# Performance work log

Measured on AMD Instinct MI355X. Metric: run time of the kernel, lower is better.

The kernel has to match this reference:

```python
import jax, jax.numpy as jnp
import numpy as np

B, T, F, H = 4096, 48, 64, 128


def _uniform(key, shape, stdv):
    return jax.random.uniform(key, shape, jnp.float32, -stdv, stdv)


def setup_inputs() -> dict:
    key = jax.random.key(0)
    ks = jax.random.split(key, 24)
    values = jax.random.normal(ks[0], (B, T, F), jnp.float32)
    masks = (jax.random.uniform(ks[1], (B, T, F)) < 0.8).astype(jnp.float32)
    deltas = jax.random.uniform(ks[2], (B, T, F), jnp.float32)
    sH = 1.0 / np.sqrt(H)
    sF = 1.0 / np.sqrt(F)
    inp = {
        "values": values, "masks": masks, "deltas": deltas,
        # TemporalDecay h: W [H, F], b [H] (stdv = 1/sqrt(out=H))
        "Wdh": _uniform(ks[3], (H, F), sH), "bdh": _uniform(ks[4], (H,), sH),
        # TemporalDecay x (diag): W [F, F], b [F]
        "Wdx": _uniform(ks[5], (F, F), sF), "bdx": _uniform(ks[6], (F,), sF),
        # hist_reg: Linear(H -> F)
        "Wh": _uniform(ks[7], (F, H), sH), "bh": _uniform(ks[8], (F,), sH),
        # feat_reg: masked F x F
        "Wf": _uniform(ks[9], (F, F), sF), "bf": _uniform(ks[10], (F,), sF),
        # weight_combine: Linear(2F -> F)
        "Wc": _uniform(ks[11], (F, 2 * F), 1.0 / np.sqrt(2 * F)),
        "bc": _uniform(ks[12], (F,), 1.0 / np.sqrt(2 * F)),
        # LSTMCell(2F -> H): gates in PyTorch order i, f, g, o
        "W_ih": _uniform(ks[13], (4 * H, 2 * F), sH),
        "W_hh": _uniform(ks[14], (4 * H, H), sH),
        "b_ih": _uniform(ks[15], (4 * H,), sH),
        "b_hh": _uniform(ks[16], (4 * H,), sH),
        # out: Linear(H -> 1)
        "Wo": _uniform(ks[17], (1, H), sH), "bo": _uniform(ks[18], (1,), sH),
    }
    return inp


def reference(values, masks, deltas, Wdh, bdh, Wdx, bdx, Wh, bh, Wf, bf,
              Wc, bc, W_ih, W_hh, b_ih, b_hh, Wo, bo):
    impute_weight = 1.0
    b, t, f = values.shape
    h_dim = Wdh.shape[0]
    eye = jnp.eye(f, dtype=values.dtype)
    Wdx_m = Wdx * eye            # diagonal temporal decay
    Wf_m = Wf * (1.0 - eye)

    def step(carry, xt):
        h, c, loss = carry
        x, m, d = xt  # each [B, F]
        gamma_h = jnp.exp(-jax.nn.relu(d @ Wdh.T + bdh))        # [B, H]
        gamma_x = jnp.exp(-jax.nn.relu(d @ Wdx_m.T + bdx))      # [B, F]
        h = h * gamma_h
        x_h = h @ Wh.T + bh
        denom = jnp.sum(m) + 1e-5
        loss = loss + jnp.sum(jnp.abs(x - x_h) * m) / denom
        x_c = m * x + (1.0 - m) * x_h
        z_h = x_c @ Wf_m.T + bf
        loss = loss + jnp.sum(jnp.abs(x - z_h) * m) / denom
        alpha = jnp.concatenate([gamma_x, m], axis=1) @ Wc.T + bc
        c_h = alpha * z_h + (1.0 - alpha) * x_h
        loss = loss + jnp.sum(jnp.abs(x - c_h) * m) / denom
        c_c = m * x + (1.0 - m) * c_h
        inputs = jnp.concatenate([c_c, m], axis=1)  # [B, 2F]
        gates = inputs @ W_ih.T + b_ih + h @ W_hh.T + b_hh
        i_g, f_g, g_g, o_g = jnp.split(gates, 4, axis=1)
        c = jax.nn.sigmoid(f_g) * c + jax.nn.sigmoid(i_g) * jnp.tanh(g_g)
        h = jax.nn.sigmoid(o_g) * jnp.tanh(c)
        return (h, c, loss), c_c

    init = (jnp.zeros((b, h_dim), values.dtype),
            jnp.zeros((b, h_dim), values.dtype),
            jnp.zeros((), values.dtype))
    xs = (jnp.swapaxes(values, 0, 1),
          jnp.swapaxes(masks, 0, 1),
          jnp.swapaxes(deltas, 0, 1))
    (h, c, x_loss), imps = jax.lax.scan(step, init, xs)
    imputations = jnp.swapaxes(imps, 0, 1)  # [B, T, F]
    predictions = h @ Wo.T + bo             # [B, 1]
    return x_loss * impute_weight, imputations, predictions
```

## Files before the change

### kernel.cpp

```cpp
#include <hip/hip_runtime.h>
#include <hip/hip_bf16.h>
#include <math.h>

#define BB 4096
#define TT 48
#define FF 64
#define HH 128
#define ROWS 16
#define NT 1024
#define NBLK (BB / ROWS)

typedef __attribute__((ext_vector_type(8))) short short8;
typedef __attribute__((ext_vector_type(4))) float f32x4;

#define MFMA(a, b, c) __builtin_amdgcn_mfma_f32_16x16x32_bf16((a), (b), (c), 0, 0, 0)

__device__ __forceinline__ float sigm(float x) { return 1.f / (1.f + __expf(-x)); }
__device__ __forceinline__ float tanh_f(float x) { return 2.f / (1.f + __expf(-2.f * x)) - 1.f; }

__global__ __launch_bounds__(256) void prep_kernel(
    const float* __restrict__ W_ih, const float* __restrict__ W_hh,
    const float* __restrict__ Wdh,  const float* __restrict__ Wh,
    const float* __restrict__ Wf,   const float* __restrict__ Wc,
    __hip_bfloat16* __restrict__ frags) {
    const int idx = blockIdx.x * 256 + threadIdx.x;
    float v;
    if (idx < 131072) {
        const int jj = idx & 7;
        const int lane = (idx >> 3) & 63;
        const int ks = (idx >> 9) & 7;
        const int tile = idx >> 12;
        const int n = tile * 16 + (lane & 15);
        const int k = ks * 32 + ((lane >> 4) << 3) + jj;
        v = (k < 128) ? W_ih[n * 128 + k] : W_hh[n * 128 + (k - 128)];
    } else {
        const int u = idx - 131072;
        const int jj = u & 7;
        const int lane = (u >> 3) & 63;
        const int lq = lane & 15, q8 = (lane >> 4) << 3;
        if (u < 8192) {
            const int ks = (u >> 9) & 1, nt = u >> 10;
            const int n = nt * 16 + lq, k = ks * 32 + q8 + jj;
            v = Wdh[n * 64 + k];
        } else if (u < 16384) {
            const int uu = u - 8192;
            const int ks = (uu >> 9) & 3, nt = uu >> 11;
            const int n = nt * 16 + lq, k = ks * 32 + q8 + jj;
            v = Wh[n * 128 + k];
        } else if (u < 20480) {
            const int uu = u - 16384;
            const int ks = (uu >> 9) & 1, nt = uu >> 10;
            const int n = nt * 16 + lq, k = ks * 32 + q8 + jj;
            v = (k == n) ? 0.f : Wf[n * 64 + k];
        } else {
            const int uu = u - 20480;
            const int ks = (uu >> 9) & 3, nt = uu >> 11;
            const int n = nt * 16 + lq, k = ks * 32 + q8 + jj;
            v = Wc[n * 128 + k];
        }
    }
    frags[idx] = __float2bfloat16(v);
}

__global__ __launch_bounds__(256) void denom1_kernel(const float* __restrict__ masks,
                                                     float* __restrict__ partials) {
    const int t = blockIdx.x >> 5;
    const int s = blockIdx.x & 31;
    const int tid = threadIdx.x;
    float acc = 0.f;
    #pragma unroll
    for (int k = 0; k < 8; ++k) {
        const int i = k * 256 + tid;
        const int b = s * 128 + (i >> 4);
        const int f = (i & 15) << 2;
        const float4 v = *(const float4*)&masks[((size_t)b * TT + t) * FF + f];
        acc += v.x + v.y + v.z + v.w;
    }
    #pragma unroll
    for (int off = 32; off; off >>= 1) acc += __shfl_down(acc, off, 64);
    __shared__ float red[4];
    if ((tid & 63) == 0) red[tid >> 6] = acc;
    __syncthreads();
    if (tid == 0) partials[blockIdx.x] = red[0] + red[1] + red[2] + red[3];
}

__global__ __launch_bounds__(64) void denom2_kernel(const float* __restrict__ partials,
                                                    float* __restrict__ inv_denom) {
    const int t = threadIdx.x;
    if (t < TT) {
        float s = 0.f;
        #pragma unroll
        for (int i = 0; i < 32; ++i) s += partials[t * 32 + i];
        inv_denom[t] = 1.f / (s + 1e-5f);
    }
}

__global__ __launch_bounds__(NT) void rits_kernel(
    const float* __restrict__ values, const float* __restrict__ masks,
    const float* __restrict__ deltas,
    const float* __restrict__ Wdx, const float* __restrict__ bdx,
    const float* __restrict__ bdh, const float* __restrict__ bh,
    const float* __restrict__ bf,  const float* __restrict__ bc,
    const float* __restrict__ b_ih, const float* __restrict__ b_hh,
    const float* __restrict__ Wo,  const float* __restrict__ bo,
    const __hip_bfloat16* __restrict__ frags,
    const float* __restrict__ inv_denom,
    float* __restrict__ ws_lossblk,
    float* __restrict__ out_imp, float* __restrict__ out_pred)
{
    __shared__ short8 whh_frag[8192];
    __shared__ __hip_bfloat16 dbuf[ROWS][72];
    __shared__ __hip_bfloat16 gxbuf[ROWS][72];
    __shared__ __hip_bfloat16 mbuf[ROWS][72];
    __shared__ __hip_bfloat16 xcbuf[ROWS][72];
    __shared__ __hip_bfloat16 ccbuf[ROWS][72];
    __shared__ __hip_bfloat16 hbufB[ROWS][136];
    __shared__ float x_lds[ROWS][65];
    __shared__ float m_lds[ROWS][65];
    __shared__ float albuf[ROWS][68];
    __shared__ float redl[16];

    const int tid = threadIdx.x;
    const int bid = blockIdx.x;
    const int b0 = bid * ROWS;
    const int lane = tid & 63;
    const int wv = tid >> 6;
    const int quad = lane >> 4;
    const int lq = lane & 15;

    const short8* f8 = (const short8*)frags;

    for (int i = tid; i < 8192; i += NT) {
        const int slot = i >> 6, ln = i & 63;
        const int g = slot >> 5, rem = slot & 31, j = rem >> 2, kk = rem & 3;
        whh_frag[i] = f8[(((g * 8 + j) * 8 + 4 + kk) << 6) + ln];
    }
    for (int i = tid; i < ROWS * 136; i += NT) ((unsigned short*)hbufB)[i] = 0;
    __syncthreads();

    float loss_acc = 0.f;

    if (wv < 8) {
        const int j_ln = wv * 16 + lq;
        const float bdh_w = bdh[j_ln];
        const float bI = b_ih[j_ln]       + b_hh[j_ln];
        const float bF = b_ih[128 + j_ln] + b_hh[128 + j_ln];
        const float bG = b_ih[256 + j_ln] + b_hh[256 + j_ln];
        const float bO = b_ih[384 + j_ln] + b_hh[384 + j_ln];
        short8 Bgam[2];
        #pragma unroll
        for (int ks = 0; ks < 2; ++ks) Bgam[ks] = f8[16384 + ((wv * 2 + ks) << 6) + lane];
        const int wbase = (wv << 8) + lane;
        const int gbase = (wv << 9) + lane;

        float c_reg[4], h_reg[4];
        #pragma unroll
        for (int r = 0; r < 4; ++r) { c_reg[r] = 0.f; h_reg[r] = 0.f; }

        __syncthreads();
        for (int t = 0; t < TT; ++t) {
            short8 Bm[4][2];
            #pragma unroll
            for (int g = 0; g < 4; ++g)
                #pragma unroll
                for (int kk = 0; kk < 2; ++kk)
                    Bm[g][kk] = f8[gbase + (g << 12) + ((2 + kk) << 6)];
            f32x4 gacc0 = {0.f,0.f,0.f,0.f}, gacc1 = {0.f,0.f,0.f,0.f};
            f32x4 gacc2 = {0.f,0.f,0.f,0.f}, gacc3 = {0.f,0.f,0.f,0.f};
            #pragma unroll
            for (int kk = 0; kk < 4; ++kk) {
                const short8 a = *(const short8*)&hbufB[lq][kk * 32 + quad * 8];
                gacc0 = MFMA(a, whh_frag[wbase + 0    + kk * 64], gacc0);
                gacc1 = MFMA(a, whh_frag[wbase + 2048 + kk * 64], gacc1);
                gacc2 = MFMA(a, whh_frag[wbase + 4096 + kk * 64], gacc2);
                gacc3 = MFMA(a, whh_frag[wbase + 6144 + kk * 64], gacc3);
            }
            __syncthreads();

            short8 Bcc[4][2];
            #pragma unroll
            for (int g = 0; g < 4; ++g)
                #pragma unroll
                for (int kk = 0; kk < 2; ++kk)
                    Bcc[g][kk] = f8[gbase + (g << 12) + (kk << 6)];
            #pragma unroll
            for (int kk = 0; kk < 2; ++kk) {
                const short8 a = *(const short8*)&mbuf[lq][kk * 32 + quad * 8];
                gacc0 = MFMA(a, Bm[0][kk], gacc0);
                gacc1 = MFMA(a, Bm[1][kk], gacc1);
                gacc2 = MFMA(a, Bm[2][kk], gacc2);
                gacc3 = MFMA(a, Bm[3][kk], gacc3);
            }
            __syncthreads();

            f32x4 ga = {0.f,0.f,0.f,0.f};
            #pragma unroll
            for (int ks = 0; ks < 2; ++ks) {
                const short8 a = *(const short8*)&dbuf[lq][ks * 32 + quad * 8];
                ga = MFMA(a, Bgam[ks], ga);
            }
            #pragma unroll
            for (int kk = 0; kk < 2; ++kk) {
                const short8 a = *(const short8*)&ccbuf[lq][kk * 32 + quad * 8];
                gacc0 = MFMA(a, Bcc[0][kk], gacc0);
                gacc1 = MFMA(a, Bcc[1][kk], gacc1);
                gacc2 = MFMA(a, Bcc[2][kk], gacc2);
                gacc3 = MFMA(a, Bcc[3][kk], gacc3);
            }
            #pragma unroll
            for (int r = 0; r < 4; ++r) {
                const float ig = sigm(gacc0[r] + bI);
                const float fg = sigm(gacc1[r] + bF);
                const float gg = tanh_f(gacc2[r] + bG);
                const float og = sigm(gacc3[r] + bO);
                c_reg[r] = fmaf(fg, c_reg[r], ig * gg);
                h_reg[r] = og * tanh_f(c_reg[r]);
                const float gh = __expf(-fmaxf(ga[r] + bdh_w, 0.f));
                hbufB[quad * 4 + r][j_ln] = __float2bfloat16(h_reg[r] * gh);
            }
            __syncthreads();
        }
        #pragma unroll
        for (int r = 0; r < 4; ++r)
            hbufB[quad * 4 + r][j_ln] = __float2bfloat16(h_reg[r]);

    } else if (wv < 12) {
        const int cw = wv - 8;
        const int f46 = (wv & 3) * 16 + lq;
        const float bh_f = bh[f46];
        const float bf_f = bf[f46];
        short8 Bxh[4], Bzh[2];
        #pragma unroll
        for (int ks = 0; ks < 4; ++ks) Bxh[ks] = f8[17408 + (((wv & 3) * 4 + ks) << 6) + lane];
        #pragma unroll
        for (int ks = 0; ks < 2; ++ks) Bzh[ks] = f8[18432 + (((wv & 3) * 2 + ks) << 6) + lane];
        const float wdx_l = Wdx[lane * (FF + 1)];
        const float bdx_l = bdx[lane];
        const int base0 = ((b0 + cw) * TT) * FF + lane;
        const int base1 = ((b0 + cw + 8) * TT) * FF + lane;
        const int imp0  = ((b0 + quad * 4) * TT) * FF + f46;

        float xn0 = values[base0], mn0 = masks[base0], dn0 = deltas[base0];
        float xn1 = values[base1], mn1 = masks[base1], dn1 = deltas[base1];
        x_lds[cw][lane] = xn0; m_lds[cw][lane] = mn0;
        gxbuf[cw][lane] = __float2bfloat16(__expf(-fmaxf(fmaf(dn0, wdx_l, bdx_l), 0.f)));
        mbuf[cw][lane]  = __float2bfloat16(mn0);
        x_lds[cw + 8][lane] = xn1; m_lds[cw + 8][lane] = mn1;
        gxbuf[cw + 8][lane] = __float2bfloat16(__expf(-fmaxf(fmaf(dn1, wdx_l, bdx_l), 0.f)));
        mbuf[cw + 8][lane]  = __float2bfloat16(mn1);

        __syncthreads();
        for (int t = 0; t < TT; ++t) {
            const float invd = inv_denom[t];
            {
                const int tn = (t < TT - 1) ? t + 1 : t;
                const int o0 = base0 + tn * FF, o1 = base1 + tn * FF;
                xn0 = values[o0]; mn0 = masks[o0]; dn0 = deltas[o0];
                xn1 = values[o1]; mn1 = masks[o1]; dn1 = deltas[o1];
            }
            f32x4 xacc = {0.f,0.f,0.f,0.f};
            #pragma unroll
            for (int ks = 0; ks < 4; ++ks) {
                const short8 a = *(const short8*)&hbufB[lq][ks * 32 + quad * 8];
                xacc = MFMA(a, Bxh[ks], xacc);
            }
            float xh_r[4];
            float stepsum = 0.f;
            #pragma unroll
            for (int r = 0; r < 4; ++r) {
                const int row = quad * 4 + r;
                const float xh = xacc[r] + bh_f;
                xh_r[r] = xh;
                const float xv = x_lds[row][f46], mv = m_lds[row][f46];
                stepsum += mv * fabsf(xv - xh);
                xcbuf[row][f46] = __float2bfloat16(fmaf(mv, xv, (1.f - mv) * xh));
            }
            __syncthreads();

            f32x4 acc5 = {0.f,0.f,0.f,0.f};
            #pragma unroll
            for (int ks = 0; ks < 2; ++ks) {
                const short8 a = *(const short8*)&xcbuf[lq][ks * 32 + quad * 8];
                acc5 = MFMA(a, Bzh[ks], acc5);
            }
            dbuf[cw][lane]     = __float2bfloat16(dn0);
            dbuf[cw + 8][lane] = __float2bfloat16(dn1);
            #pragma unroll
            for (int r = 0; r < 4; ++r) {
                const int row = quad * 4 + r;
                const float zh = acc5[r] + bf_f;
                const float xv = x_lds[row][f46], mv = m_lds[row][f46];
                stepsum += mv * fabsf(xv - zh);
                const float alpha = albuf[row][f46];
                const float ch = fmaf(alpha, zh, (1.f - alpha) * xh_r[r]);
                stepsum += mv * fabsf(xv - ch);
                const float cc = fmaf(mv, xv, (1.f - mv) * ch);
                ccbuf[row][f46] = __float2bfloat16(cc);
                out_imp[imp0 + r * (TT * FF) + t * FF] = cc;
            }
            loss_acc = fmaf(stepsum, invd, loss_acc);
            __syncthreads();

            x_lds[cw][lane] = xn0; m_lds[cw][lane] = mn0;
            gxbuf[cw][lane] = __float2bfloat16(__expf(-fmaxf(fmaf(dn0, wdx_l, bdx_l), 0.f)));
            mbuf[cw][lane]  = __float2bfloat16(mn0);
            x_lds[cw + 8][lane] = xn1; m_lds[cw + 8][lane] = mn1;
            gxbuf[cw + 8][lane] = __float2bfloat16(__expf(-fmaxf(fmaf(dn1, wdx_l, bdx_l), 0.f)));
            mbuf[cw + 8][lane]  = __float2bfloat16(mn1);
            __syncthreads();
        }

    } else {
        const int cw = wv - 8;
        const int f46 = (wv & 3) * 16 + lq;
        const float bc_f = bc[f46];
        short8 Bal[4];
        #pragma unroll
        for (int ks = 0; ks < 4; ++ks) Bal[ks] = f8[18944 + (((wv & 3) * 4 + ks) << 6) + lane];
        const float wdx_l = Wdx[lane * (FF + 1)];
        const float bdx_l = bdx[lane];
        const int base0 = ((b0 + cw) * TT) * FF + lane;
        const int base1 = ((b0 + cw + 8) * TT) * FF + lane;

        float xn0 = values[base0], mn0 = masks[base0], dn0 = deltas[base0];
        float xn1 = values[base1], mn1 = masks[base1], dn1 = deltas[base1];
        x_lds[cw][lane] = xn0; m_lds[cw][lane] = mn0;
        gxbuf[cw][lane] = __float2bfloat16(__expf(-fmaxf(fmaf(dn0, wdx_l, bdx_l), 0.f)));
        mbuf[cw][lane]  = __float2bfloat16(mn0);
        x_lds[cw + 8][lane] = xn1; m_lds[cw + 8][lane] = mn1;
        gxbuf[cw + 8][lane] = __float2bfloat16(__expf(-fmaxf(fmaf(dn1, wdx_l, bdx_l), 0.f)));
        mbuf[cw + 8][lane]  = __float2bfloat16(mn1);

        __syncthreads();
        for (int t = 0; t < TT; ++t) {
            {
                const int tn = (t < TT - 1) ? t + 1 : t;
                const int o0 = base0 + tn * FF, o1 = base1 + tn * FF;
                xn0 = values[o0]; mn0 = masks[o0]; dn0 = deltas[o0];
                xn1 = values[o1]; mn1 = masks[o1]; dn1 = deltas[o1];
            }
            f32x4 aa = {0.f,0.f,0.f,0.f};
            #pragma unroll
            for (int ks = 0; ks < 2; ++ks) {
                const short8 a = *(const short8*)&gxbuf[lq][ks * 32 + quad * 8];
                aa = MFMA(a, Bal[ks], aa);
            }
            #pragma unroll
            for (int ks = 2; ks < 4; ++ks) {
                const short8 a = *(const short8*)&mbuf[lq][(ks - 2) * 32 + quad * 8];
                aa = MFMA(a, Bal[ks], aa);
            }
            #pragma unroll
            for (int r = 0; r < 4; ++r)
                albuf[quad * 4 + r][f46] = aa[r] + bc_f;
            __syncthreads();

            dbuf[cw][lane]     = __float2bfloat16(dn0);
            dbuf[cw + 8][lane] = __float2bfloat16(dn1);
            __syncthreads();

            x_lds[cw][lane] = xn0; m_lds[cw][lane] = mn0;
            gxbuf[cw][lane] = __float2bfloat16(__expf(-fmaxf(fmaf(dn0, wdx_l, bdx_l), 0.f)));
            mbuf[cw][lane]  = __float2bfloat16(mn0);
            x_lds[cw + 8][lane] = xn1; m_lds[cw + 8][lane] = mn1;
            gxbuf[cw + 8][lane] = __float2bfloat16(__expf(-fmaxf(fmaf(dn1, wdx_l, bdx_l), 0.f)));
            mbuf[cw + 8][lane]  = __float2bfloat16(mn1);
            __syncthreads();
        }
    }

    __syncthreads();
    if (tid < 512) {
        const int r = tid >> 5, l = tid & 31;
        float s = 0.f;
        #pragma unroll
        for (int k = l; k < HH; k += 32) s += __bfloat162float(hbufB[r][k]) * Wo[k];
        #pragma unroll
        for (int off = 16; off; off >>= 1) s += __shfl_down(s, off, 32);
        if (l == 0) out_pred[b0 + r] = s + bo[0];
    }
    #pragma unroll
    for (int off = 32; off; off >>= 1) loss_acc += __shfl_down(loss_acc, off, 64);
    if (lane == 0) redl[wv] = loss_acc;
    __syncthreads();
    if (tid == 0) {
        float s = 0.f;
        #pragma unroll
        for (int w = 0; w < 16; ++w) s += redl[w];
        ws_lossblk[bid] = s;
    }
}

__global__ __launch_bounds__(256) void final_kernel(const float* __restrict__ ws_lossblk,
                                                    float* __restrict__ out_loss) {
    const int tid = threadIdx.x;
    float s = ws_lossblk[tid];
    #pragma unroll
    for (int off = 32; off; off >>= 1) s += __shfl_down(s, off, 64);
    __shared__ float red[4];
    if ((tid & 63) == 0) red[tid >> 6] = s;
    __syncthreads();
    if (tid == 0) out_loss[0] = red[0] + red[1] + red[2] + red[3];
}

extern "C" void kernel_launch(void* const* d_in, const int* in_sizes, int n_in,
                              void* d_out, int out_size, void* d_ws, size_t ws_size,
                              hipStream_t stream) {
    const float* values = (const float*)d_in[0];
    const float* masks  = (const float*)d_in[1];
    const float* deltas = (const float*)d_in[2];
    const float* Wdh  = (const float*)d_in[3];
    const float* bdh  = (const float*)d_in[4];
    const float* Wdx  = (const float*)d_in[5];
    const float* bdx  = (const float*)d_in[6];
    const float* Wh   = (const float*)d_in[7];
    const float* bh   = (const float*)d_in[8];
    const float* Wf   = (const float*)d_in[9];
    const float* bf   = (const float*)d_in[10];
    const float* Wc   = (const float*)d_in[11];
    const float* bc   = (const float*)d_in[12];
    const float* W_ih = (const float*)d_in[13];
    const float* W_hh = (const float*)d_in[14];
    const float* b_ih = (const float*)d_in[15];
    const float* b_hh = (const float*)d_in[16];
    const float* Wo   = (const float*)d_in[17];
    const float* bo   = (const float*)d_in[18];

    __hip_bfloat16* frags = (__hip_bfloat16*)d_ws;
    float* inv_denom  = (float*)((char*)d_ws + 320 * 1024);
    float* partials   = inv_denom + 64;
    float* ws_lossblk = partials + 2048;

    float* out_loss = (float*)d_out;
    float* out_imp  = out_loss + 1;
    float* out_pred = out_imp + (size_t)BB * TT * FF;

    prep_kernel<<<624, 256, 0, stream>>>(W_ih, W_hh, Wdh, Wh, Wf, Wc, frags);
    denom1_kernel<<<TT * 32, 256, 0, stream>>>(masks, partials);
    denom2_kernel<<<1, 64, 0, stream>>>(partials, inv_denom);
    rits_kernel<<<NBLK, NT, 0, stream>>>(
        values, masks, deltas, Wdx, bdx, bdh, bh, bf, bc,
        b_ih, b_hh, Wo, bo, frags, inv_denom, ws_lossblk, out_imp, out_pred);
    final_kernel<<<1, 256, 0, stream>>>(ws_lossblk, out_loss);
}
```

Baseline: 320.6 us.

## Merge prep and denominator kernels, defer loss normalization, register-cache half of W_hh

```diff
diff --git a/kernel.cpp b/kernel.cpp
--- a/kernel.cpp
+++ b/kernel.cpp
@@ -18,80 +18,70 @@
 __device__ __forceinline__ float sigm(float x) { return 1.f / (1.f + __expf(-x)); }
 __device__ __forceinline__ float tanh_f(float x) { return 2.f / (1.f + __expf(-2.f * x)) - 1.f; }
 
-__global__ __launch_bounds__(256) void prep_kernel(
+__global__ __launch_bounds__(256) void prep_denom_kernel(
     const float* __restrict__ W_ih, const float* __restrict__ W_hh,
     const float* __restrict__ Wdh,  const float* __restrict__ Wh,
     const float* __restrict__ Wf,   const float* __restrict__ Wc,
-    __hip_bfloat16* __restrict__ frags) {
-    const int idx = blockIdx.x * 256 + threadIdx.x;
-    float v;
-    if (idx < 131072) {
-        const int jj = idx & 7;
-        const int lane = (idx >> 3) & 63;
-        const int ks = (idx >> 9) & 7;
-        const int tile = idx >> 12;
-        const int n = tile * 16 + (lane & 15);
-        const int k = ks * 32 + ((lane >> 4) << 3) + jj;
-        v = (k < 128) ? W_ih[n * 128 + k] : W_hh[n * 128 + (k - 128)];
+    __hip_bfloat16* __restrict__ frags,
+    const float* __restrict__ masks, float* __restrict__ partials) {
+    const int tid = threadIdx.x;
+    if (blockIdx.x < 624) {
+        const int idx = blockIdx.x * 256 + tid;
+        float v;
+        if (idx < 131072) {
+            const int jj = idx & 7;
+            const int lane = (idx >> 3) & 63;
+            const int ks = (idx >> 9) & 7;
+            const int tile = idx >> 12;
+            const int n = tile * 16 + (lane & 15);
+            const int k = ks * 32 + ((lane >> 4) << 3) + jj;
+            v = (k < 128) ? W_ih[n * 128 + k] : W_hh[n * 128 + (k - 128)];
+        } else {
+            const int u = idx - 131072;
+            const int jj = u & 7;
+            const int lane = (u >> 3) & 63;
+            const int lq = lane & 15, q8 = (lane >> 4) << 3;
+            if (u < 8192) {
+                const int ks = (u >> 9) & 1, nt = u >> 10;
+                const int n = nt * 16 + lq, k = ks * 32 + q8 + jj;
+                v = Wdh[n * 64 + k];
+            } else if (u < 16384) {
+                const int uu = u - 8192;
+                const int ks = (uu >> 9) & 3, nt = uu >> 11;
+                const int n = nt * 16 + lq, k = ks * 32 + q8 + jj;
+                v = Wh[n * 128 + k];
+            } else if (u < 20480) {
+                const int uu = u - 16384;
+                const int ks = (uu >> 9) & 1, nt = uu >> 10;
+                const int n = nt * 16 + lq, k = ks * 32 + q8 + jj;
+                v = (k == n) ? 0.f : Wf[n * 64 + k];
+            } else {
+                const int uu = u - 20480;
+                const int ks = (uu >> 9) & 3, nt = uu >> 11;
+                const int n = nt * 16 + lq, k = ks * 32 + q8 + jj;
+                v = Wc[n * 128 + k];
+            }
+        }
+        frags[idx] = __float2bfloat16(v);
     } else {
-        const int u = idx - 131072;
-        const int jj = u & 7;
-        const int lane = (u >> 3) & 63;
-        const int lq = lane & 15, q8 = (lane >> 4) << 3;
-        if (u < 8192) {
-            const int ks = (u >> 9) & 1, nt = u >> 10;
-            const int n = nt * 16 + lq, k = ks * 32 + q8 + jj;
-            v = Wdh[n * 64 + k];
-        } else if (u < 16384) {
-            const int uu = u - 8192;
-            const int ks = (uu >> 9) & 3, nt = uu >> 11;
-            const int n = nt * 16 + lq, k = ks * 32 + q8 + jj;
-            v = Wh[n * 128 + k];
-        } else if (u < 20480) {
-            const int uu = u - 16384;
-            const int ks = (uu >> 9) & 1, nt = uu >> 10;
-            const int n = nt * 16 + lq, k = ks * 32 + q8 + jj;
-            v = (k == n) ? 0.f : Wf[n * 64 + k];
-        } else {
-            const int uu = u - 20480;
-            const int ks = (uu >> 9) & 3, nt = uu >> 11;
-            const int n = nt * 16 + lq, k = ks * 32 + q8 + jj;
-            v = Wc[n * 128 + k];
-        }
-    }
-    frags[idx] = __float2bfloat16(v);
-}
-
-__global__ __launch_bounds__(256) void denom1_kernel(const float* __restrict__ masks,
-                                                     float* __restrict__ partials) {
-    const int t = blockIdx.x >> 5;
-    const int s = blockIdx.x & 31;
-    const int tid = threadIdx.x;
-    float acc = 0.f;
-    #pragma unroll
-    for (int k = 0; k < 8; ++k) {
-        const int i = k * 256 + tid;
-        const int b = s * 128 + (i >> 4);
-        const int f = (i & 15) << 2;
-        const float4 v = *(const float4*)&masks[((size_t)b * TT + t) * FF + f];
-        acc += v.x + v.y + v.z + v.w;
-    }
-    #pragma unroll
-    for (int off = 32; off; off >>= 1) acc += __shfl_down(acc, off, 64);
-    __shared__ float red[4];
-    if ((tid & 63) == 0) red[tid >> 6] = acc;
-    __syncthreads();
-    if (tid == 0) partials[blockIdx.x] = red[0] + red[1] + red[2] + red[3];
-}
-
-__global__ __launch_bounds__(64) void denom2_kernel(const float* __restrict__ partials,
-                                                    float* __restrict__ inv_denom) {
-    const int t = threadIdx.x;
-    if (t < TT) {
-        float s = 0.f;
-        #pragma unroll
-        for (int i = 0; i < 32; ++i) s += partials[t * 32 + i];
-        inv_denom[t] = 1.f / (s + 1e-5f);
+        const int b = blockIdx.x - 624;
+        const int t = b >> 5;
+        const int s = b & 31;
+        float acc = 0.f;
+        #pragma unroll
+        for (int k = 0; k < 8; ++k) {
+            const int i = k * 256 + tid;
+            const int bb = s * 128 + (i >> 4);
+            const int f = (i & 15) << 2;
+            const float4 v = *(const float4*)&masks[((size_t)bb * TT + t) * FF + f];
+            acc += v.x + v.y + v.z + v.w;
+        }
+        #pragma unroll
+        for (int off = 32; off; off >>= 1) acc += __shfl_down(acc, off, 64);
+        __shared__ float red[4];
+        if ((tid & 63) == 0) red[tid >> 6] = acc;
+        __syncthreads();
+        if (tid == 0) partials[b] = red[0] + red[1] + red[2] + red[3];
     }
 }
 
@@ -104,11 +94,10 @@
     const float* __restrict__ b_ih, const float* __restrict__ b_hh,
     const float* __restrict__ Wo,  const float* __restrict__ bo,
     const __hip_bfloat16* __restrict__ frags,
-    const float* __restrict__ inv_denom,
-    float* __restrict__ ws_lossblk,
+    float* __restrict__ ws_numer,
     float* __restrict__ out_imp, float* __restrict__ out_pred)
 {
-    __shared__ short8 whh_frag[8192];
+    __shared__ short8 whh_frag[4096];
     __shared__ __hip_bfloat16 dbuf[ROWS][72];
     __shared__ __hip_bfloat16 gxbuf[ROWS][72];
     __shared__ __hip_bfloat16 mbuf[ROWS][72];
@@ -118,7 +107,7 @@
     __shared__ float x_lds[ROWS][65];
     __shared__ float m_lds[ROWS][65];
     __shared__ float albuf[ROWS][68];
-    __shared__ float redl[16];
+    __shared__ float lts[4][TT];
 
     const int tid = threadIdx.x;
     const int bid = blockIdx.x;
@@ -130,15 +119,13 @@
 
     const short8* f8 = (const short8*)frags;
 
-    for (int i = tid; i < 8192; i += NT) {
+    for (int i = tid; i < 4096; i += NT) {
         const int slot = i >> 6, ln = i & 63;
-        const int g = slot >> 5, rem = slot & 31, j = rem >> 2, kk = rem & 3;
-        whh_frag[i] = f8[(((g * 8 + j) * 8 + 4 + kk) << 6) + ln];
+        const int g2 = slot >> 5, rem = slot & 31, j = rem >> 2, kk = rem & 3;
+        whh_frag[i] = f8[((((g2 + 2) * 8 + j) * 8 + 4 + kk) << 6) + ln];
     }
     for (int i = tid; i < ROWS * 136; i += NT) ((unsigned short*)hbufB)[i] = 0;
     __syncthreads();
-
-    float loss_acc = 0.f;
 
     if (wv < 8) {
         const int j_ln = wv * 16 + lq;
@@ -153,6 +140,13 @@
         const int wbase = (wv << 8) + lane;
         const int gbase = (wv << 9) + lane;
 
+        short8 WhI[4], WhF[4];
+        #pragma unroll
+        for (int kk = 0; kk < 4; ++kk) {
+            WhI[kk] = f8[gbase + (0 << 12) + ((4 + kk) << 6)];
+            WhF[kk] = f8[gbase + (1 << 12) + ((4 + kk) << 6)];
+        }
+
         float c_reg[4], h_reg[4];
         #pragma unroll
         for (int r = 0; r < 4; ++r) { c_reg[r] = 0.f; h_reg[r] = 0.f; }
@@ -170,10 +164,10 @@
             #pragma unroll
             for (int kk = 0; kk < 4; ++kk) {
                 const short8 a = *(const short8*)&hbufB[lq][kk * 32 + quad * 8];
-                gacc0 = MFMA(a, whh_frag[wbase + 0    + kk * 64], gacc0);
-                gacc1 = MFMA(a, whh_frag[wbase + 2048 + kk * 64], gacc1);
-                gacc2 = MFMA(a, whh_frag[wbase + 4096 + kk * 64], gacc2);
-                gacc3 = MFMA(a, whh_frag[wbase + 6144 + kk * 64], gacc3);
+                gacc0 = MFMA(a, WhI[kk], gacc0);
+                gacc1 = MFMA(a, WhF[kk], gacc1);
+                gacc2 = MFMA(a, whh_frag[wbase + 0    + kk * 64], gacc2);
+                gacc3 = MFMA(a, whh_frag[wbase + 2048 + kk * 64], gacc3);
             }
             __syncthreads();
 
@@ -251,7 +245,6 @@
 
         __syncthreads();
         for (int t = 0; t < TT; ++t) {
-            const float invd = inv_denom[t];
             {
                 const int tn = (t < TT - 1) ? t + 1 : t;
                 const int o0 = base0 + tn * FF, o1 = base1 + tn * FF;
@@ -264,7 +257,7 @@
                 const short8 a = *(const short8*)&hbufB[lq][ks * 32 + quad * 8];
                 xacc = MFMA(a, Bxh[ks], xacc);
             }
-            float xh_r[4];
+            float xh_r[4], xv_r[4], mv_r[4];
             float stepsum = 0.f;
             #pragma unroll
             for (int r = 0; r < 4; ++r) {
@@ -272,6 +265,7 @@
                 const float xh = xacc[r] + bh_f;
                 xh_r[r] = xh;
                 const float xv = x_lds[row][f46], mv = m_lds[row][f46];
+                xv_r[r] = xv; mv_r[r] = mv;
                 stepsum += mv * fabsf(xv - xh);
                 xcbuf[row][f46] = __float2bfloat16(fmaf(mv, xv, (1.f - mv) * xh));
             }
@@ -289,16 +283,17 @@
             for (int r = 0; r < 4; ++r) {
                 const int row = quad * 4 + r;
                 const float zh = acc5[r] + bf_f;
-                const float xv = x_lds[row][f46], mv = m_lds[row][f46];
-                stepsum += mv * fabsf(xv - zh);
+                stepsum += mv_r[r] * fabsf(xv_r[r] - zh);
                 const float alpha = albuf[row][f46];
                 const float ch = fmaf(alpha, zh, (1.f - alpha) * xh_r[r]);
-                stepsum += mv * fabsf(xv - ch);
-                const float cc = fmaf(mv, xv, (1.f - mv) * ch);
+                stepsum += mv_r[r] * fabsf(xv_r[r] - ch);
+                const float cc = fmaf(mv_r[r], xv_r[r], (1.f - mv_r[r]) * ch);
                 ccbuf[row][f46] = __float2bfloat16(cc);
                 out_imp[imp0 + r * (TT * FF) + t * FF] = cc;
             }
-            loss_acc = fmaf(stepsum, invd, loss_acc);
+            #pragma unroll
+            for (int off = 32; off; off >>= 1) stepsum += __shfl_down(stepsum, off, 64);
+            if (lane == 0) lts[cw][t] = stepsum;
             __syncthreads();
 
             x_lds[cw][lane] = xn0; m_lds[cw][lane] = mn0;
@@ -379,26 +374,30 @@
         for (int off = 16; off; off >>= 1) s += __shfl_down(s, off, 32);
         if (l == 0) out_pred[b0 + r] = s + bo[0];
     }
-    #pragma unroll
-    for (int off = 32; off; off >>= 1) loss_acc += __shfl_down(loss_acc, off, 64);
-    if (lane == 0) redl[wv] = loss_acc;
-    __syncthreads();
-    if (tid == 0) {
-        float s = 0.f;
-        #pragma unroll
-        for (int w = 0; w < 16; ++w) s += redl[w];
-        ws_lossblk[bid] = s;
-    }
+    if (tid < TT)
+        ws_numer[tid * NBLK + bid] = lts[0][tid] + lts[1][tid] + lts[2][tid] + lts[3][tid];
 }
 
-__global__ __launch_bounds__(256) void final_kernel(const float* __restrict__ ws_lossblk,
+__global__ __launch_bounds__(256) void final_kernel(const float* __restrict__ partials,
+                                                    const float* __restrict__ ws_numer,
                                                     float* __restrict__ out_loss) {
     const int tid = threadIdx.x;
-    float s = ws_lossblk[tid];
-    #pragma unroll
-    for (int off = 32; off; off >>= 1) s += __shfl_down(s, off, 64);
+    const int lane = tid & 63, wv = tid >> 6;
     __shared__ float red[4];
-    if ((tid & 63) == 0) red[tid >> 6] = s;
+    float acc = 0.f;
+    for (int t = wv; t < TT; t += 4) {
+        float ns = 0.f;
+        #pragma unroll
+        for (int q = 0; q < 4; ++q) ns += ws_numer[t * NBLK + lane * 4 + q];
+        float ds = (lane < 32) ? partials[t * 32 + lane] : 0.f;
+        #pragma unroll
+        for (int off = 32; off; off >>= 1) {
+            ns += __shfl_down(ns, off, 64);
+            ds += __shfl_down(ds, off, 64);
+        }
+        if (lane == 0) acc += ns / (ds + 1e-5f);
+    }
+    if (lane == 0) red[wv] = acc;
     __syncthreads();
     if (tid == 0) out_loss[0] = red[0] + red[1] + red[2] + red[3];
 }
@@ -427,19 +426,17 @@
     const float* bo   = (const float*)d_in[18];
 
     __hip_bfloat16* frags = (__hip_bfloat16*)d_ws;
-    float* inv_denom  = (float*)((char*)d_ws + 320 * 1024);
-    float* partials   = inv_denom + 64;
-    float* ws_lossblk = partials + 2048;
+    float* partials = (float*)((char*)d_ws + 320 * 1024);
+    float* ws_numer = partials + 2048;
 
     float* out_loss = (float*)d_out;
     float* out_imp  = out_loss + 1;
     float* out_pred = out_imp + (size_t)BB * TT * FF;
 
-    prep_kernel<<<624, 256, 0, stream>>>(W_ih, W_hh, Wdh, Wh, Wf, Wc, frags);
-    denom1_kernel<<<TT * 32, 256, 0, stream>>>(masks, partials);
-    denom2_kernel<<<1, 64, 0, stream>>>(partials, inv_denom);
+    prep_denom_kernel<<<2160, 256, 0, stream>>>(
+        W_ih, W_hh, Wdh, Wh, Wf, Wc, frags, masks, partials);
     rits_kernel<<<NBLK, NT, 0, stream>>>(
         values, masks, deltas, Wdx, bdx, bdh, bh, bf, bc,
-        b_ih, b_hh, Wo, bo, frags, inv_denom, ws_lossblk, out_imp, out_pred);
-    final_kernel<<<1, 256, 0, stream>>>(ws_lossblk, out_loss);
+        b_ih, b_hh, Wo, bo, frags, ws_numer, out_imp, out_pred);
+    final_kernel<<<1, 256, 0, stream>>>(partials, ws_numer, out_loss);
 }
```

After: 390.7 us. +21.9%, slower.
